# Kernel optimization log

Hardware: AMD Instinct MI355X
Metric: run time of the kernel (lower is better)

The kernel has to match this reference:

```python
import jax, jax.numpy as jnp
from jax import lax
import numpy as np

M_FILTERS = 128   # rows of responses D
N_CHANNELS = 1024 # cols of responses D (spectral channels)
BATCH = 4096
N_LAYERS = 17
IMAX = 50


def setup_inputs() -> dict:
    key = jax.random.key(0)
    k1, k2, k3, k4 = jax.random.split(key, 4)
    t1 = jax.random.normal(k1, (BATCH, N_CHANNELS), dtype=jnp.float32)
    t2 = jax.random.normal(k2, (BATCH, N_CHANNELS), dtype=jnp.float32)
    params = jax.random.uniform(k3, (M_FILTERS, N_LAYERS), dtype=jnp.float32)
    responses = jax.random.normal(k4, (M_FILTERS, N_CHANNELS), dtype=jnp.float32)
    return {
        "t1": t1,
        "t2": t2,
        "params": params,
        "thick_min": jnp.float32(0.0),
        "thick_max": jnp.float32(1.0),
        "beta_range": jnp.float32(0.1),
        "responses": responses,
    }


def _coherence_reduce(D0):
    """Faithful vectorized version of the 50-iteration coherence-reduction loop.

    The original per-row Python loop (Ri[i] > Rth branch) only reads row i and
    pre-computed Rth/delta, so it is exactly a masked row update.
    torch.linalg.eig on the symmetric matrices G is replaced by eigh (same
    eigenpairs up to sign/order; order is fixed by the explicit descending sort,
    and only the top-M eigenpairs reach the output D[:M,:]).
    """
    Mr, Nr = D0.shape
    ratio = jnp.float32(Nr / Mr)
    eye_b = jnp.eye(Nr, dtype=bool)

    def body(_, D):
        D = D / jnp.linalg.norm(D)                      # Frobenius norm over (0,1)
        G = D.T @ D                                     # [N, N]
        Sigma, V = jnp.linalg.eigh(G)
        Sigma = jnp.where(jnp.abs(Sigma) > 1e-10, ratio, Sigma)
        G = (V * Sigma[None, :]) @ V.T                  # V diag(Sigma) V^T
        G0 = jnp.abs(G - jnp.diag(jnp.diag(G)))
        Ri = jnp.sum(G0, axis=0)                        # [N]
        Rth = jnp.min(Ri)
        delta = Rth / (Nr - 1)
        mask = (Ri > Rth)[:, None]                      # rows to clip
        Gn = jnp.where(mask, delta * jnp.sign(G), G)
        Gn = jnp.where(eye_b, G, Gn)                    # keep original diagonal
        G = (Gn + Gn.T) * 0.5
        Sigma, V = jnp.linalg.eigh(G)
        order = jnp.argsort(-Sigma)                     # descending
        Sigma = Sigma[order]
        V = V[:, order]
        # Original: Sigma[M:-1]=0 then D = diag(Sigma)^{1/2} @ V.T, D = D[:M,:].
        # Only the top-M eigenpairs contribute to the first M rows.
        Dn = jnp.power(Sigma[:Mr], 0.5)[:, None] * V[:, :Mr].T  # [M, N]
        return Dn

    return lax.fori_loop(0, IMAX, body, D0)


def reference(t1, t2, params, thick_min, thick_max, beta_range, responses):
    # HybnetLoss: MSE match loss + hinge range loss (filter_loss is zeroed in source)
    match_loss = jnp.mean((t1 - t2) ** 2)
    d = jnp.float32(0.01)
    res = jnp.maximum((params - thick_min - d) / (-d),
                      (params - thick_max + d) / d)
    range_loss = jnp.mean(jnp.maximum(res, jnp.zeros_like(res)))
    original_loss = match_loss + beta_range * range_loss

    # HybnetLoss_plus: coherence-reduction regularizer on the response matrix
    D = _coherence_reduce(responses)
    rloss = jnp.mean((D - responses) ** 2)
    return original_loss + rloss
```

## Files before the change

kernel.cpp:

```cpp
#include <hip/hip_runtime.h>

#define NBLK 256
#define NTHR 512

#define OFF_G    0
#define OFF_QT   1048576
#define OFF_Y    1179648
#define OFF_C    1703936
#define OFF_RP   1851392
#define OFF_ACC  1867776
#define OFF_BAR  1867792

#define BAR_A 0
#define BAR_B 64
#define BAR_C 128
#define BAR_E 136

typedef float v4f __attribute__((ext_vector_type(4)));

__device__ __forceinline__ void cld4_8(v4f& a, v4f& b, v4f& c, v4f& d,
                                       v4f& e, v4f& f, v4f& g, v4f& h,
                                       const float* pa, const float* pb,
                                       const float* pc, const float* pd,
                                       const float* pe, const float* pf,
                                       const float* pg, const float* ph) {
    asm volatile("global_load_dwordx4 %0, %8, off sc1\n\t"
                 "global_load_dwordx4 %1, %9, off sc1\n\t"
                 "global_load_dwordx4 %2, %10, off sc1\n\t"
                 "global_load_dwordx4 %3, %11, off sc1\n\t"
                 "global_load_dwordx4 %4, %12, off sc1\n\t"
                 "global_load_dwordx4 %5, %13, off sc1\n\t"
                 "global_load_dwordx4 %6, %14, off sc1\n\t"
                 "global_load_dwordx4 %7, %15, off sc1\n\t"
                 "s_waitcnt vmcnt(0)"
                 : "=&v"(a), "=&v"(b), "=&v"(c), "=&v"(d),
                   "=&v"(e), "=&v"(f), "=&v"(g), "=&v"(h)
                 : "v"(pa), "v"(pb), "v"(pc), "v"(pd),
                   "v"(pe), "v"(pf), "v"(pg), "v"(ph) : "memory");
}
__device__ __forceinline__ void cld4_4(v4f& a, v4f& b, v4f& c, v4f& d,
                                       const float* pa, const float* pb,
                                       const float* pc, const float* pd) {
    asm volatile("global_load_dwordx4 %0, %4, off sc1\n\t"
                 "global_load_dwordx4 %1, %5, off sc1\n\t"
                 "global_load_dwordx4 %2, %6, off sc1\n\t"
                 "global_load_dwordx4 %3, %7, off sc1\n\t"
                 "s_waitcnt vmcnt(0)"
                 : "=&v"(a), "=&v"(b), "=&v"(c), "=&v"(d)
                 : "v"(pa), "v"(pb), "v"(pc), "v"(pd) : "memory");
}
__device__ __forceinline__ void cld4_2(v4f& a, v4f& b,
                                       const float* pa, const float* pb) {
    asm volatile("global_load_dwordx4 %0, %2, off sc1\n\t"
                 "global_load_dwordx4 %1, %3, off sc1\n\t"
                 "s_waitcnt vmcnt(0)"
                 : "=&v"(a), "=&v"(b) : "v"(pa), "v"(pb) : "memory");
}
__device__ __forceinline__ void cld1_4(float& a, float& b, float& c, float& d,
                                       const float* pa, const float* pb,
                                       const float* pc, const float* pd) {
    asm volatile("global_load_dword %0, %4, off sc1\n\t"
                 "global_load_dword %1, %5, off sc1\n\t"
                 "global_load_dword %2, %6, off sc1\n\t"
                 "global_load_dword %3, %7, off sc1\n\t"
                 "s_waitcnt vmcnt(0)"
                 : "=&v"(a), "=&v"(b), "=&v"(c), "=&v"(d)
                 : "v"(pa), "v"(pb), "v"(pc), "v"(pd) : "memory");
}
__device__ __forceinline__ void cld1_8(float& a, float& b, float& c, float& d,
                                       float& e, float& f, float& g, float& h,
                                       const float* pa, const float* pb,
                                       const float* pc, const float* pd,
                                       const float* pe, const float* pf,
                                       const float* pg, const float* ph) {
    asm volatile("global_load_dword %0, %8, off sc1\n\t"
                 "global_load_dword %1, %9, off sc1\n\t"
                 "global_load_dword %2, %10, off sc1\n\t"
                 "global_load_dword %3, %11, off sc1\n\t"
                 "global_load_dword %4, %12, off sc1\n\t"
                 "global_load_dword %5, %13, off sc1\n\t"
                 "global_load_dword %6, %14, off sc1\n\t"
                 "global_load_dword %7, %15, off sc1\n\t"
                 "s_waitcnt vmcnt(0)"
                 : "=&v"(a), "=&v"(b), "=&v"(c), "=&v"(d),
                   "=&v"(e), "=&v"(f), "=&v"(g), "=&v"(h)
                 : "v"(pa), "v"(pb), "v"(pc), "v"(pd),
                   "v"(pe), "v"(pf), "v"(pg), "v"(ph) : "memory");
}
__device__ __forceinline__ void iss2(v4f& a, v4f& b,
                                     const float* pa, const float* pb) {
    asm volatile("global_load_dwordx4 %0, %2, off sc1\n\t"
                 "global_load_dwordx4 %1, %3, off sc1"
                 : "=&v"(a), "=&v"(b) : "v"(pa), "v"(pb) : "memory");
}
__device__ __forceinline__ void wt2(v4f& a, v4f& b) {
    asm volatile("s_waitcnt vmcnt(0)" : "+v"(a), "+v"(b) :: "memory");
}
__device__ __forceinline__ void iss1(v4f& a, const float* pa) {
    asm volatile("global_load_dwordx4 %0, %1, off sc1"
                 : "=&v"(a) : "v"(pa) : "memory");
}
__device__ __forceinline__ void wt1(v4f& a) {
    asm volatile("s_waitcnt vmcnt(0)" : "+v"(a) :: "memory");
}

__device__ __forceinline__ void ast2(float* p, float a, float b) {
    union { unsigned long long u; float f[2]; } c; c.f[0] = a; c.f[1] = b;
    __hip_atomic_store((unsigned long long*)p, c.u,
                       __ATOMIC_RELAXED, __HIP_MEMORY_SCOPE_AGENT);
}
__device__ __forceinline__ float ald(const float* p) {
    return __hip_atomic_load(p, __ATOMIC_RELAXED, __HIP_MEMORY_SCOPE_AGENT);
}
__device__ __forceinline__ void ast(float* p, float x) {
    __hip_atomic_store(p, x, __ATOMIC_RELAXED, __HIP_MEMORY_SCOPE_AGENT);
}

__device__ __forceinline__ void bar_arrive(unsigned* bb, int line) {
    __syncthreads();
    if (threadIdx.x == 0)
        __hip_atomic_fetch_add(bb + line * 16, 1u,
                               __ATOMIC_RELAXED, __HIP_MEMORY_SCOPE_AGENT);
}
__device__ __forceinline__ void bar_wait(unsigned* bb, int wbase, int nlines,
                                         unsigned tgt) {
    if ((int)threadIdx.x < nlines) {
        while (__hip_atomic_load(bb + (wbase + threadIdx.x) * 16,
                                 __ATOMIC_RELAXED, __HIP_MEMORY_SCOPE_AGENT) < tgt)
            __builtin_amdgcn_s_sleep(1);
    }
    __builtin_amdgcn_s_waitcnt(0);
    __syncthreads();
}

union Smem {
    struct { float As[32][68]; float Bs[32][68]; float Rs[64][17]; } gg;
    struct { float Cs[128][129]; float inv_d[16]; float irs[128];
             float Xs[16][64]; } chol;
    struct { float Ri[1024]; float red[512]; float As[32][36]; float Bs[32][68]; } gy;
    struct { float As[32][68]; float Bs[32][68]; float red[512]; } tb;
    float red[512];
};

__device__ __forceinline__ void dev_match(Smem* sm, const float* t1, const float* t2,
                                          float* accb, int w) {
    int tid = threadIdx.x;
    const float4* a = (const float4*)t1;
    const float4* b = (const float4*)t2;
    float s = 0.f;
    for (int i = w * 512 + tid; i < 1048576; i += 218 * 512) {
        float4 x = a[i], y = b[i];
        float d0 = x.x - y.x, d1 = x.y - y.y, d2 = x.z - y.z, d3 = x.w - y.w;
        s += d0 * d0 + d1 * d1 + d2 * d2 + d3 * d3;
    }
    sm->red[tid] = s; __syncthreads();
    for (int w2 = 256; w2 > 0; w2 >>= 1) {
        if (tid < w2) sm->red[tid] += sm->red[tid + w2];
        __syncthreads();
    }
    if (tid == 0) atomicAdd(&accb[0], sm->red[0]);
    __syncthreads();
}

__device__ __forceinline__ void dev_range(Smem* sm, const float* params, const float* tmin,
                                          const float* tmax, float* accb) {
    int tid = threadIdx.x;
    float a = tmin[0], b = tmax[0];
    const float d = 0.01f;
    float s = 0.f;
    for (int i = tid; i < 128 * 17; i += 512) {
        float p = params[i];
        float r1 = (p - a - d) / (-d);
        float r2 = (p - b + d) / d;
        s += fmaxf(fmaxf(r1, r2), 0.f);
    }
    sm->red[tid] = s; __syncthreads();
    for (int w = 256; w > 0; w >>= 1) {
        if (tid < w) sm->red[tid] += sm->red[tid + w];
        __syncthreads();
    }
    if (tid == 0) atomicAdd(&accb[1], sm->red[0]);
    __syncthreads();
}

__device__ __forceinline__ void dev_sumsq(Smem* sm, const float* X, float* accb, int w) {
    int tid = threadIdx.x;
    float s = 0.f;
    for (int i = w * 512 + tid; i < 131072; i += 2048) { float v = X[i]; s += v * v; }
    sm->red[tid] = s; __syncthreads();
    for (int w2 = 256; w2 > 0; w2 >>= 1) {
        if (tid < w2) sm->red[tid] += sm->red[tid + w2];
        __syncthreads();
    }
    if (tid == 0) atomicAdd(&accb[3], sm->red[0]);
    __syncthreads();
}

__device__ __forceinline__ void dev_syrk(Smem* sm, const float* A, const float* B,
                                         float* C, int bid) {
    int tid = threadIdx.x;
    int q0 = (bid & 1) * 64, p0 = ((bid >> 1) & 1) * 64, z = bid >> 2;
    int kc0 = z * 128;
    int p = tid & 63, kg = (tid >> 6) * 4;
    int tx = tid & 15, ty = tid >> 4;
    float acc[2][4] = {};
    v4f av, bv;
    iss2(av, bv, &A[(p0 + p) * 1024 + kc0 + kg], &B[(q0 + p) * 1024 + kc0 + kg]);
    for (int ck = 0; ck < 4; ++ck) {
        wt2(av, bv);
        sm->gg.As[kg + 0][p] = av.x; sm->gg.As[kg + 1][p] = av.y;
        sm->gg.As[kg + 2][p] = av.z; sm->gg.As[kg + 3][p] = av.w;
        sm->gg.Bs[kg + 0][p] = bv.x; sm->gg.Bs[kg + 1][p] = bv.y;
        sm->gg.Bs[kg + 2][p] = bv.z; sm->gg.Bs[kg + 3][p] = bv.w;
        __syncthreads();
        if (ck < 3) {
            int kn = kc0 + (ck + 1) * 32 + kg;
            iss2(av, bv, &A[(p0 + p) * 1024 + kn], &B[(q0 + p) * 1024 + kn]);
        }
        for (int k = 0; k < 32; ++k) {
            float2 a2 = *(const float2*)&sm->gg.As[k][ty * 2];
            float4 b4 = *(const float4*)&sm->gg.Bs[k][tx * 4];
            acc[0][0] += a2.x * b4.x; acc[0][1] += a2.x * b4.y;
            acc[0][2] += a2.x * b4.z; acc[0][3] += a2.x * b4.w;
            acc[1][0] += a2.y * b4.x; acc[1][1] += a2.y * b4.y;
            acc[1][2] += a2.y * b4.z; acc[1][3] += a2.y * b4.w;
        }
        __syncthreads();
    }
    #pragma unroll
    for (int i = 0; i < 2; ++i)
        #pragma unroll
        for (int j = 0; j < 4; ++j)
            atomicAdd(&C[(p0 + ty * 2 + i) * 128 + q0 + tx * 4 + j], acc[i][j]);
}

__device__ __forceinline__ void dev_cholTrsm(Smem* sm, const float* C, const float* RHS,
                                             float* Qt, int bid) {
    int tid = threadIdx.x;
    {
        const float* base = C + tid * 32;
        v4f z0, z1, z2, z3, z4, z5, z6, z7;
        cld4_8(z0, z1, z2, z3, z4, z5, z6, z7,
               base, base + 4, base + 8, base + 12,
               base + 16, base + 20, base + 24, base + 28);
        int r = tid >> 2, c0 = (tid & 3) * 32;
        *(v4f*)&sm->chol.Cs[r][c0]      = z0; *(v4f*)&sm->chol.Cs[r][c0 + 4]  = z1;
        *(v4f*)&sm->chol.Cs[r][c0 + 8]  = z2; *(v4f*)&sm->chol.Cs[r][c0 + 12] = z3;
        *(v4f*)&sm->chol.Cs[r][c0 + 16] = z4; *(v4f*)&sm->chol.Cs[r][c0 + 20] = z5;
        *(v4f*)&sm->chol.Cs[r][c0 + 24] = z6; *(v4f*)&sm->chol.Cs[r][c0 + 28] = z7;
    }
    __syncthreads();
    int lane = tid & 63;
    for (int kb = 0; kb < 8; ++kb) {
        int k0 = kb * 16;
        if (tid < 64) {
            float P0[16], P1[16], invs[16];
            #pragma unroll
            for (int u = 0; u < 16; ++u) {
                P0[u] = sm->chol.Cs[lane][k0 + u];
                P1[u] = sm->chol.Cs[lane + 64][k0 + u];
            }
            #pragma unroll
            for (int kk = 0; kk < 16; ++kk) {
                int k = k0 + kk;
                int src = k & 63;
                bool hi = (k >= 64);
                float pr[16];
                #pragma unroll
                for (int u = 0; u < 16; ++u)
                    if (u >= kk) pr[u] = __shfl(hi ? P1[u] : P0[u], src);
                float inv = 1.0f / pr[kk];
                invs[kk] = inv;
                float f0 = (lane > k) ? P0[kk] * inv : 0.f;
                float f1 = ((lane + 64) > k) ? P1[kk] * inv : 0.f;
                #pragma unroll
                for (int u = kk + 1; u < 16; ++u) {
                    P0[u] -= f0 * pr[u];
                    P1[u] -= f1 * pr[u];
                }
            }
            #pragma unroll
            for (int u = 0; u < 16; ++u) {
                sm->chol.Cs[lane][k0 + u] = P0[u];
                sm->chol.Cs[lane + 64][k0 + u] = P1[u];
            }
            if (lane == 0) {
                #pragma unroll
                for (int kk = 0; kk < 16; ++kk) sm->chol.inv_d[kk] = invs[kk];
            }
        }
        __syncthreads();
        int base = k0 + 16;
        if (base < 128) {
            int hh = tid >> 6, cc = tid & 63;
            int j1 = base + cc;
            int j2 = base + cc + 64;
            bool has1 = (j1 < 128), has2 = (j2 < 128);
            float w1[16], w2[16];
            if (has1) {
                #pragma unroll
                for (int u = 0; u < 16; ++u) w1[u] = sm->chol.Cs[j1][k0 + u] * sm->chol.inv_d[u];
            }
            if (has2) {
                #pragma unroll
                for (int u = 0; u < 16; ++u) w2[u] = sm->chol.Cs[j2][k0 + u] * sm->chol.inv_d[u];
            }
            int rlo = hh * 16;
            int istart = rlo > base ? rlo : base;
            for (int i = istart; i < rlo + 16; ++i) {
                float v[16];
                #pragma unroll
                for (int u = 0; u < 16; ++u) v[u] = sm->chol.Cs[i][k0 + u];
                float a1 = 0.f, a2 = 0.f;
                #pragma unroll
                for (int u = 0; u < 16; ++u) { a1 += v[u] * w1[u]; a2 += v[u] * w2[u]; }
                if (has1) sm->chol.Cs[i][j1] -= a1;
                if (has2) sm->chol.Cs[i][j2] -= a2;
            }
        }
        __syncthreads();
    }
    if (tid < 128) sm->chol.irs[tid] = 1.0f / sqrtf(sm->chol.Cs[tid][tid]);
    int c = tid & 63, h = tid >> 6;
    int j0 = bid * 64;
    float acc[16];
    {
        const float* p = &RHS[(h * 16) * 1024 + j0 + c];
        cld1_8(acc[0], acc[1], acc[2], acc[3], acc[4], acc[5], acc[6], acc[7],
               p, p + 1024, p + 2048, p + 3072, p + 4096, p + 5120, p + 6144, p + 7168);
        cld1_8(acc[8], acc[9], acc[10], acc[11], acc[12], acc[13], acc[14], acc[15],
               p + 8192, p + 9216, p + 10240, p + 11264,
               p + 12288, p + 13312, p + 14336, p + 15360);
    }
    __syncthreads();
    for (int pb = 0; pb < 8; ++pb) {
        int p0 = pb * 16;
        if (h == pb) {
            #pragma unroll
            for (int kk = 0; kk < 16; ++kk) {
                int k = p0 + kk;
                float irsk = sm->chol.irs[k];
                float x = acc[kk] * irsk;
                acc[kk] = x;
                sm->chol.Xs[kk][c] = x;
                float xs = x * irsk;
                #pragma unroll
                for (int r = kk + 1; r < 16; ++r)
                    acc[r] -= sm->chol.Cs[p0 + r][k] * xs;
            }
        }
        __syncthreads();
        if (h > pb) {
            int rb = h * 16;
            #pragma unroll
            for (int kk = 0; kk < 16; ++kk) {
                int k = p0 + kk;
                float xs = sm->chol.Xs[kk][c] * sm->chol.irs[k];
                #pragma unroll
                for (int r = 0; r < 16; ++r)
                    acc[r] -= sm->chol.Cs[rb + r][k] * xs;
            }
        }
        __syncthreads();
    }
    #pragma unroll
    for (int r = 0; r < 16; ++r)
        ast(&Qt[(h * 16 + r) * 1024 + j0 + c], acc[r]);
}

__device__ __forceinline__ void dev_gemmG(Smem* sm, const float* Qt, float* G,
                                          float* Rpart, int bid) {
    int tid = threadIdx.x;
    int tx = tid & 15, ty = tid >> 4;
    int bx = bid & 15, by = bid >> 4;
    int a0 = by * 64, b0 = bx * 64;
    int r0 = tid >> 4, c4 = (tid & 15) << 2;
    float acc[2][4] = {};
    v4f av, bv;
    iss2(av, bv, &Qt[r0 * 1024 + a0 + c4], &Qt[r0 * 1024 + b0 + c4]);
    for (int kc = 0; kc < 128; kc += 32) {
        wt2(av, bv);
        *(v4f*)&sm->gg.As[r0][c4] = av;
        *(v4f*)&sm->gg.Bs[r0][c4] = bv;
        __syncthreads();
        if (kc < 96) {
            int kn = kc + 32;
            iss2(av, bv, &Qt[(kn + r0) * 1024 + a0 + c4],
                 &Qt[(kn + r0) * 1024 + b0 + c4]);
        }
        for (int k = 0; k < 32; ++k) {
            float2 a2 = *(const float2*)&sm->gg.As[k][ty * 2];
            float4 b4 = *(const float4*)&sm->gg.Bs[k][tx * 4];
            acc[0][0] += a2.x * b4.x; acc[0][1] += a2.x * b4.y;
            acc[0][2] += a2.x * b4.z; acc[0][3] += a2.x * b4.w;
            acc[1][0] += a2.y * b4.x; acc[1][1] += a2.y * b4.y;
            acc[1][2] += a2.y * b4.z; acc[1][3] += a2.y * b4.w;
        }
        __syncthreads();
    }
    float rsum[2] = {0.f, 0.f};
    #pragma unroll
    for (int i = 0; i < 2; ++i) {
        int aa = a0 + ty * 2 + i;
        float g[4];
        #pragma unroll
        for (int j = 0; j < 4; ++j) g[j] = 8.f * acc[i][j];
        float* gp = &G[aa * 1024 + b0 + tx * 4];
        ast2(gp, g[0], g[1]);
        ast2(gp + 2, g[2], g[3]);
        int bb = b0 + tx * 4;
        #pragma unroll
        for (int j = 0; j < 4; ++j) rsum[i] += (aa == bb + j) ? 0.f : fabsf(g[j]);
    }
    sm->gg.Rs[ty * 2 + 0][tx] = rsum[0];
    sm->gg.Rs[ty * 2 + 1][tx] = rsum[1];
    __syncthreads();
    if (tid < 64) {
        float s = 0.f;
        #pragma unroll
        for (int x = 0; x < 16; ++x) s += sm->gg.Rs[tid][x];
        ast(&Rpart[(a0 + tid) * 16 + bx], s);
    }
}

__device__ __forceinline__ void dev_ri(Smem* sm, const float* Rpart,
                                       float* rth, float* delta) {
    int tid = threadIdx.x;
    int e0 = tid, e1 = tid + 512;
    v4f t0, t1, t2, t3, u0, u1, u2, u3;
    cld4_8(t0, t1, t2, t3, u0, u1, u2, u3,
           &Rpart[e0 * 16], &Rpart[e0 * 16 + 4],
           &Rpart[e0 * 16 + 8], &Rpart[e0 * 16 + 12],
           &Rpart[e1 * 16], &Rpart[e1 * 16 + 4],
           &Rpart[e1 * 16 + 8], &Rpart[e1 * 16 + 12]);
    float s0 = 0.f;
    s0 += t0.x; s0 += t0.y; s0 += t0.z; s0 += t0.w;
    s0 += t1.x; s0 += t1.y; s0 += t1.z; s0 += t1.w;
    s0 += t2.x; s0 += t2.y; s0 += t2.z; s0 += t2.w;
    s0 += t3.x; s0 += t3.y; s0 += t3.z; s0 += t3.w;
    float s1 = 0.f;
    s1 += u0.x; s1 += u0.y; s1 += u0.z; s1 += u0.w;
    s1 += u1.x; s1 += u1.y; s1 += u1.z; s1 += u1.w;
    s1 += u2.x; s1 += u2.y; s1 += u2.z; s1 += u2.w;
    s1 += u3.x; s1 += u3.y; s1 += u3.z; s1 += u3.w;
    sm->gy.Ri[e0] = s0;
    sm->gy.Ri[e1] = s1;
    float mn = fminf(s0, s1);
    #pragma unroll
    for (int off = 32; off > 0; off >>= 1)
        mn = fminf(mn, __shfl_xor(mn, off));
    if ((tid & 63) == 0) sm->gy.red[tid >> 6] = mn;
    __syncthreads();
    float r = sm->gy.red[0];
    #pragma unroll
    for (int w = 1; w < 8; ++w) r = fminf(r, sm->gy.red[w]);
    *rth = r;
    *delta = r / 1023.f;
}

__device__ __forceinline__ void dev_gemmY(Smem* sm, const float* Qt, const float* G,
                                          float rth, float delta, float* Y, int bid) {
    int tid = threadIdx.x;
    int j0 = (bid & 15) * 64;
    int m0 = ((bid >> 4) & 3) * 32;
    int kz = bid >> 6;
    int kc0 = kz * 256;
    int tx = tid & 15, ty = tid >> 4;
    int m = (tid & 255) >> 3, k4 = (tid & 7) << 2;
    int rg = tid >> 4, cg = (tid & 15) << 2;
    float acc[4] = {};
    v4f q, g0;
    if (tid < 256) iss1(q, &Qt[(m0 + m) * 1024 + kc0 + k4]);
    iss1(g0, &G[(kc0 + rg) * 1024 + j0 + cg]);
    for (int kc = kc0; kc < kc0 + 256; kc += 32) {
        wt1(g0);
        if (tid < 256) {
            wt1(q);
            *(v4f*)&sm->gy.As[m][k4] = q;
        }
        {
            int a = kc + rg;
            float ria = sm->gy.Ri[a];
            v4f bw;
            #pragma unroll
            for (int u = 0; u < 4; ++u) {
                int b = j0 + cg + u;
                float g = g0[u];
                float sg = delta * ((g > 0.f) ? 1.f : ((g < 0.f) ? -1.f : 0.f));
                float ga = (ria > rth) ? sg : g;
                float gb = (sm->gy.Ri[b] > rth) ? sg : g;
                bw[u] = (a == b) ? g : 0.5f * (ga + gb);
            }
            *(v4f*)&sm->gy.Bs[rg][cg] = bw;
        }
        __syncthreads();
        if (kc < kc0 + 224) {
            int kn = kc + 32;
            if (tid < 256) iss1(q, &Qt[(m0 + m) * 1024 + kn + k4]);
            iss1(g0, &G[(kn + rg) * 1024 + j0 + cg]);
        }
        #pragma unroll
        for (int kb = 0; kb < 8; ++kb) {
            v4f qa = *(const v4f*)&sm->gy.As[ty][kb * 4];
            #pragma unroll
            for (int kk = 0; kk < 4; ++kk) {
                float4 b4 = *(const float4*)&sm->gy.Bs[kb * 4 + kk][tx * 4];
                float a = qa[kk];
                acc[0] += a * b4.x; acc[1] += a * b4.y;
                acc[2] += a * b4.z; acc[3] += a * b4.w;
            }
        }
        __syncthreads();
    }
    #pragma unroll
    for (int j = 0; j < 4; ++j)
        atomicAdd(&Y[(m0 + ty) * 1024 + j0 + tx * 4 + j], acc[j]);
}

__device__ __forceinline__ void dev_trB(Smem* sm, const float* Qt, const float* G,
                                        const float* Rpart, float* accb, int bid) {
    int tid = threadIdx.x;
    float rth, delta;
    dev_ri(sm, Rpart, &rth, &delta);
    __syncthreads();
    int tx = tid & 15, ty = tid >> 4;
    int a0 = (bid >> 4) * 64, b0 = (bid & 15) * 64;
    int r0 = tid >> 4, c4 = (tid & 15) << 2;
    float acc[2][4] = {};
    for (int kc = 0; kc < 128; kc += 32) {
        v4f av, bv;
        cld4_2(av, bv, &Qt[(kc + r0) * 1024 + a0 + c4],
               &Qt[(kc + r0) * 1024 + b0 + c4]);
        *(v4f*)&sm->tb.As[r0][c4] = av;
        *(v4f*)&sm->tb.Bs[r0][c4] = bv;
        __syncthreads();
        for (int k = 0; k < 32; ++k) {
            float2 a2 = *(const float2*)&sm->tb.As[k][ty * 2];
            float4 b4 = *(const float4*)&sm->tb.Bs[k][tx * 4];
            acc[0][0] += a2.x * b4.x; acc[0][1] += a2.x * b4.y;
            acc[0][2] += a2.x * b4.z; acc[0][3] += a2.x * b4.w;
            acc[1][0] += a2.y * b4.x; acc[1][1] += a2.y * b4.y;
            acc[1][2] += a2.y * b4.z; acc[1][3] += a2.y * b4.w;
        }
        __syncthreads();
    }
    float rib[4];
    #pragma unroll
    for (int j = 0; j < 4; ++j) {
        int bb = b0 + tx * 4 + j;
        v4f t0, t1, t2, t3;
        cld4_4(t0, t1, t2, t3, &Rpart[bb * 16], &Rpart[bb * 16 + 4],
               &Rpart[bb * 16 + 8], &Rpart[bb * 16 + 12]);
        float s = 0.f;
        s += t0.x; s += t0.y; s += t0.z; s += t0.w;
        s += t1.x; s += t1.y; s += t1.z; s += t1.w;
        s += t2.x; s += t2.y; s += t2.z; s += t2.w;
        s += t3.x; s += t3.y; s += t3.z; s += t3.w;
        rib[j] = s;
    }
    float s = 0.f;
    #pragma unroll
    for (int i = 0; i < 2; ++i) {
        int aa = a0 + ty * 2 + i;
        v4f t0, t1, t2, t3;
        cld4_4(t0, t1, t2, t3, &Rpart[aa * 16], &Rpart[aa * 16 + 4],
               &Rpart[aa * 16 + 8], &Rpart[aa * 16 + 12]);
        float ria = 0.f;
        ria += t0.x; ria += t0.y; ria += t0.z; ria += t0.w;
        ria += t1.x; ria += t1.y; ria += t1.z; ria += t1.w;
        ria += t2.x; ria += t2.y; ria += t2.z; ria += t2.w;
        ria += t3.x; ria += t3.y; ria += t3.z; ria += t3.w;
        float g0, g1, g2, g3;
        const float* gp = &G[aa * 1024 + b0 + tx * 4];
        cld1_4(g0, g1, g2, g3, gp, gp + 1, gp + 2, gp + 3);
        float gv[4] = {g0, g1, g2, g3};
        #pragma unroll
        for (int j = 0; j < 4; ++j) {
            int bb = b0 + tx * 4 + j;
            float g = gv[j];
            float sg = delta * ((g > 0.f) ? 1.f : ((g < 0.f) ? -1.f : 0.f));
            float ga = (ria > rth) ? sg : g;
            float gb = (rib[j] > rth) ? sg : g;
            float gp2 = (aa == bb) ? g : 0.5f * (ga + gb);
            s += gp2 * acc[i][j];
        }
    }
    __syncthreads();
    sm->tb.red[tid] = s;
    __syncthreads();
    for (int w = 256; w > 0; w >>= 1) {
        if (tid < w) sm->tb.red[tid] += sm->tb.red[tid + w];
        __syncthreads();
    }
    if (tid == 0) atomicAdd(&accb[2], sm->tb.red[0]);
}

__global__ __launch_bounds__(512) void mega(const float* __restrict__ t1,
                                            const float* __restrict__ t2,
                                            const float* __restrict__ params,
                                            const float* __restrict__ tmin,
                                            const float* __restrict__ tmax,
                                            const float* __restrict__ beta,
                                            const float* __restrict__ R,
                                            float* ws, float* out) {
    float* G     = ws + OFF_G;
    float* Qt    = ws + OFF_QT;
    float* Y     = ws + OFF_Y;
    float* C     = ws + OFF_C;
    float* Rpart = ws + OFF_RP;
    float* accb  = ws + OFF_ACC;
    unsigned* bb = (unsigned*)(ws + OFF_BAR);
    __shared__ Smem sm;
    int bid = blockIdx.x;
    int tid = threadIdx.x;
    unsigned phA = 0, phB = 0, phC = 0, phE = 0;

    if (bid < 32) {
        ast(&C[bid * 512 + tid], 0.f);
    } else if (bid < 250) dev_match(&sm, t1, t2, accb, bid - 32);
    else if (bid == 250) dev_range(&sm, params, tmin, tmax, accb);
    else if (bid < 255) dev_sumsq(&sm, R, accb, bid - 251);
    ++phC;
    if (bid < 32) {
        bar_arrive(bb, BAR_C + (bid >> 2));
        bar_wait(bb, BAR_C, 8, phC * 4);
        dev_syrk(&sm, R, R, C, bid);
    }
    ++phC;
    if (bid < 32) bar_arrive(bb, BAR_C + (bid >> 2));
    if (bid < 16) {
        bar_wait(bb, BAR_C, 8, phC * 4);
        dev_cholTrsm(&sm, C, R, Qt, bid);
    }
    ++phE;
    if (bid < 16) bar_arrive(bb, BAR_E + (bid >> 2));
    bar_wait(bb, BAR_E, 4, phE * 4);

    for (int it = 0; it < 50; ++it) {
        dev_gemmG(&sm, Qt, G, Rpart, bid);
        ast(&Y[bid * 512 + tid], 0.f);
        if (bid < 32) ast(&C[bid * 512 + tid], 0.f);
        ++phA;
        bar_arrive(bb, BAR_A + (bid & 63));
        bar_wait(bb, BAR_A, 64, phA * 4);
        {
            float rth, delta;
            dev_ri(&sm, Rpart, &rth, &delta);
            dev_gemmY(&sm, Qt, G, rth, delta, Y, bid);
        }
        ++phB;
        bar_arrive(bb, BAR_B + (bid & 63));
        if (bid < 32) {
            bar_wait(bb, BAR_B, 64, phB * 4);
            dev_syrk(&sm, Y, Y, C, bid);
        }
        ++phC;
        if (bid < 32) bar_arrive(bb, BAR_C + (bid >> 2));
        if (bid < 16) {
            bar_wait(bb, BAR_C, 8, phC * 4);
            dev_cholTrsm(&sm, C, Y, Qt, bid);
        }
        ++phE;
        if (bid < 16) bar_arrive(bb, BAR_E + (bid >> 2));
        bar_wait(bb, BAR_E, 4, phE * 4);
    }

    dev_trB(&sm, Qt, G, Rpart, accb, bid);
    ++phA;
    bar_arrive(bb, BAR_A + (bid & 63));
    if (bid == 0) {
        bar_wait(bb, BAR_A, 64, phA * 4);
        if (tid == 0)
            out[0] = ald(&accb[0]) / 4194304.f + beta[0] * (ald(&accb[1]) / 2176.f)
                   + (ald(&accb[2]) + ald(&accb[3])) / 131072.f;
    }
}

extern "C" void kernel_launch(void* const* d_in, const int* in_sizes, int n_in,
                              void* d_out, int out_size, void* d_ws, size_t ws_size,
                              hipStream_t stream) {
    const float* t1 = (const float*)d_in[0];
    const float* t2 = (const float*)d_in[1];
    const float* params = (const float*)d_in[2];
    const float* tmin = (const float*)d_in[3];
    const float* tmax = (const float*)d_in[4];
    const float* beta = (const float*)d_in[5];
    const float* R = (const float*)d_in[6];
    float* ws = (float*)d_ws;
    float* out = (float*)d_out;

    hipMemsetAsync(ws + OFF_ACC, 0, 9280, stream);
    mega<<<NBLK, NTHR, 0, stream>>>(t1, t2, params, tmin, tmax, beta, R, ws, out);
}
```

Measured before the change: 7.340 ms.

## Deepen load pipelining with double-buffered LDS and overlap Cholesky panel with updates

The syrk, gemmG and gemmY device phases now issue all four or more K-chunk global loads up front and wait on them with partial vmcnt counts. They also double-buffer the LDS tiles so that one barrier per chunk replaces two. The blocked Cholesky is restructured: the next panel factorization by wave 0 overlaps the trailing update done by the other waves, and the RHS loads are issued before factorization and waited on later. The change also uses fast rcp/rsq intrinsics and a lighter LDS-only barrier. Costs are higher register pressure and LDS footprint, plus some precision loss from the approximate reciprocals.

```diff
diff --git a/kernel.cpp b/kernel.cpp
--- a/kernel.cpp
+++ b/kernel.cpp
@@ -17,6 +17,7 @@
 #define BAR_E 136
 
 typedef float v4f __attribute__((ext_vector_type(4)));
+typedef float v2f __attribute__((ext_vector_type(2)));
 
 __device__ __forceinline__ void cld4_8(v4f& a, v4f& b, v4f& c, v4f& d,
                                        v4f& e, v4f& f, v4f& g, v4f& h,
@@ -67,12 +68,24 @@
                  : "=&v"(a), "=&v"(b), "=&v"(c), "=&v"(d)
                  : "v"(pa), "v"(pb), "v"(pc), "v"(pd) : "memory");
 }
-__device__ __forceinline__ void cld1_8(float& a, float& b, float& c, float& d,
-                                       float& e, float& f, float& g, float& h,
-                                       const float* pa, const float* pb,
-                                       const float* pc, const float* pd,
-                                       const float* pe, const float* pf,
-                                       const float* pg, const float* ph) {
+__device__ __forceinline__ void iss2(v4f& a, v4f& b,
+                                     const float* pa, const float* pb) {
+    asm volatile("global_load_dwordx4 %0, %2, off sc1\n\t"
+                 "global_load_dwordx4 %1, %3, off sc1"
+                 : "=&v"(a), "=&v"(b) : "v"(pa), "v"(pb) : "memory");
+}
+__device__ __forceinline__ void issY(v2f& q, v4f& g,
+                                     const float* pq, const float* pg) {
+    asm volatile("global_load_dwordx2 %0, %2, off sc1\n\t"
+                 "global_load_dwordx4 %1, %3, off sc1"
+                 : "=&v"(q), "=&v"(g) : "v"(pq), "v"(pg) : "memory");
+}
+__device__ __forceinline__ void issS8(float& a, float& b, float& c, float& d,
+                                      float& e, float& f, float& g, float& h,
+                                      const float* pa, const float* pb,
+                                      const float* pc, const float* pd,
+                                      const float* pe, const float* pf,
+                                      const float* pg, const float* ph) {
     asm volatile("global_load_dword %0, %8, off sc1\n\t"
                  "global_load_dword %1, %9, off sc1\n\t"
                  "global_load_dword %2, %10, off sc1\n\t"
@@ -80,28 +93,39 @@
                  "global_load_dword %4, %12, off sc1\n\t"
                  "global_load_dword %5, %13, off sc1\n\t"
                  "global_load_dword %6, %14, off sc1\n\t"
-                 "global_load_dword %7, %15, off sc1\n\t"
-                 "s_waitcnt vmcnt(0)"
+                 "global_load_dword %7, %15, off sc1"
                  : "=&v"(a), "=&v"(b), "=&v"(c), "=&v"(d),
                    "=&v"(e), "=&v"(f), "=&v"(g), "=&v"(h)
                  : "v"(pa), "v"(pb), "v"(pc), "v"(pd),
                    "v"(pe), "v"(pf), "v"(pg), "v"(ph) : "memory");
 }
-__device__ __forceinline__ void iss2(v4f& a, v4f& b,
-                                     const float* pa, const float* pb) {
-    asm volatile("global_load_dwordx4 %0, %2, off sc1\n\t"
-                 "global_load_dwordx4 %1, %3, off sc1"
-                 : "=&v"(a), "=&v"(b) : "v"(pa), "v"(pb) : "memory");
-}
-__device__ __forceinline__ void wt2(v4f& a, v4f& b) {
-    asm volatile("s_waitcnt vmcnt(0)" : "+v"(a), "+v"(b) :: "memory");
-}
-__device__ __forceinline__ void iss1(v4f& a, const float* pa) {
-    asm volatile("global_load_dwordx4 %0, %1, off sc1"
-                 : "=&v"(a) : "v"(pa) : "memory");
-}
-__device__ __forceinline__ void wt1(v4f& a) {
-    asm volatile("s_waitcnt vmcnt(0)" : "+v"(a) :: "memory");
+#define DEF_WT2(NAME, NSTR) \
+__device__ __forceinline__ void NAME(v4f& a, v4f& b) { \
+    asm volatile("s_waitcnt vmcnt(" NSTR ")" : "+v"(a), "+v"(b) :: "memory"); }
+DEF_WT2(wt2_6, "6")
+DEF_WT2(wt2_4, "4")
+DEF_WT2(wt2_2, "2")
+DEF_WT2(wt2_0, "0")
+#define DEF_WTY(NAME, NSTR) \
+__device__ __forceinline__ void NAME(v2f& q, v4f& g) { \
+    asm volatile("s_waitcnt vmcnt(" NSTR ")" : "+v"(q), "+v"(g) :: "memory"); }
+DEF_WTY(wtY_6, "6")
+DEF_WTY(wtY_4, "4")
+DEF_WTY(wtY_2, "2")
+DEF_WTY(wtY_0, "0")
+__device__ __forceinline__ void wtA16(float* a) {
+    asm volatile("s_waitcnt vmcnt(0)"
+                 : "+v"(a[0]), "+v"(a[1]), "+v"(a[2]), "+v"(a[3]),
+                   "+v"(a[4]), "+v"(a[5]), "+v"(a[6]), "+v"(a[7]),
+                   "+v"(a[8]), "+v"(a[9]), "+v"(a[10]), "+v"(a[11]),
+                   "+v"(a[12]), "+v"(a[13]), "+v"(a[14]), "+v"(a[15])
+                 :: "memory");
+}
+
+__device__ __forceinline__ void syncL() {
+    asm volatile("s_waitcnt lgkmcnt(0)" ::: "memory");
+    __builtin_amdgcn_s_barrier();
+    asm volatile("" ::: "memory");
 }
 
 __device__ __forceinline__ void ast2(float* p, float a, float b) {
@@ -134,10 +158,11 @@
 }
 
 union Smem {
-    struct { float As[32][68]; float Bs[32][68]; float Rs[64][17]; } gg;
-    struct { float Cs[128][129]; float inv_d[16]; float irs[128];
+    struct { float As[2][32][68]; float Bs[2][32][68]; float Rs[64][17]; } gg;
+    struct { float Cs[128][129]; float inv_d[2][16]; float irs[128];
              float Xs[16][64]; } chol;
-    struct { float Ri[1024]; float red[512]; float As[32][36]; float Bs[32][68]; } gy;
+    struct { float Ri[1024]; float red[512]; float As[2][32][36];
+             float Bs[2][32][68]; } gy;
     struct { float As[32][68]; float Bs[32][68]; float red[512]; } tb;
     float red[512];
 };
@@ -196,6 +221,23 @@
     __syncthreads();
 }
 
+#define SY_BODY(CK, RA, RB, WT) do { \
+    WT; \
+    sm->gg.As[(CK) & 1][kg + 0][p] = RA.x; sm->gg.As[(CK) & 1][kg + 1][p] = RA.y; \
+    sm->gg.As[(CK) & 1][kg + 2][p] = RA.z; sm->gg.As[(CK) & 1][kg + 3][p] = RA.w; \
+    sm->gg.Bs[(CK) & 1][kg + 0][p] = RB.x; sm->gg.Bs[(CK) & 1][kg + 1][p] = RB.y; \
+    sm->gg.Bs[(CK) & 1][kg + 2][p] = RB.z; sm->gg.Bs[(CK) & 1][kg + 3][p] = RB.w; \
+    syncL(); \
+    for (int k = 0; k < 32; ++k) { \
+        float2 a2 = *(const float2*)&sm->gg.As[(CK) & 1][k][ty * 2]; \
+        float4 b4 = *(const float4*)&sm->gg.Bs[(CK) & 1][k][tx * 4]; \
+        acc[0][0] += a2.x * b4.x; acc[0][1] += a2.x * b4.y; \
+        acc[0][2] += a2.x * b4.z; acc[0][3] += a2.x * b4.w; \
+        acc[1][0] += a2.y * b4.x; acc[1][1] += a2.y * b4.y; \
+        acc[1][2] += a2.y * b4.z; acc[1][3] += a2.y * b4.w; \
+    } \
+} while (0)
+
 __device__ __forceinline__ void dev_syrk(Smem* sm, const float* A, const float* B,
                                          float* C, int bid) {
     int tid = threadIdx.x;
@@ -204,34 +246,60 @@
     int p = tid & 63, kg = (tid >> 6) * 4;
     int tx = tid & 15, ty = tid >> 4;
     float acc[2][4] = {};
-    v4f av, bv;
-    iss2(av, bv, &A[(p0 + p) * 1024 + kc0 + kg], &B[(q0 + p) * 1024 + kc0 + kg]);
-    for (int ck = 0; ck < 4; ++ck) {
-        wt2(av, bv);
-        sm->gg.As[kg + 0][p] = av.x; sm->gg.As[kg + 1][p] = av.y;
-        sm->gg.As[kg + 2][p] = av.z; sm->gg.As[kg + 3][p] = av.w;
-        sm->gg.Bs[kg + 0][p] = bv.x; sm->gg.Bs[kg + 1][p] = bv.y;
-        sm->gg.Bs[kg + 2][p] = bv.z; sm->gg.Bs[kg + 3][p] = bv.w;
-        __syncthreads();
-        if (ck < 3) {
-            int kn = kc0 + (ck + 1) * 32 + kg;
-            iss2(av, bv, &A[(p0 + p) * 1024 + kn], &B[(q0 + p) * 1024 + kn]);
-        }
-        for (int k = 0; k < 32; ++k) {
-            float2 a2 = *(const float2*)&sm->gg.As[k][ty * 2];
-            float4 b4 = *(const float4*)&sm->gg.Bs[k][tx * 4];
-            acc[0][0] += a2.x * b4.x; acc[0][1] += a2.x * b4.y;
-            acc[0][2] += a2.x * b4.z; acc[0][3] += a2.x * b4.w;
-            acc[1][0] += a2.y * b4.x; acc[1][1] += a2.y * b4.y;
-            acc[1][2] += a2.y * b4.z; acc[1][3] += a2.y * b4.w;
-        }
-        __syncthreads();
-    }
+    v4f a0r, b0r, a1r, b1r, a2r, b2r, a3r, b3r;
+    const float* Ab = &A[(p0 + p) * 1024 + kc0 + kg];
+    const float* Bb = &B[(q0 + p) * 1024 + kc0 + kg];
+    iss2(a0r, b0r, Ab, Bb);
+    iss2(a1r, b1r, Ab + 32, Bb + 32);
+    iss2(a2r, b2r, Ab + 64, Bb + 64);
+    iss2(a3r, b3r, Ab + 96, Bb + 96);
+    SY_BODY(0, a0r, b0r, wt2_6(a0r, b0r));
+    SY_BODY(1, a1r, b1r, wt2_4(a1r, b1r));
+    SY_BODY(2, a2r, b2r, wt2_2(a2r, b2r));
+    SY_BODY(3, a3r, b3r, wt2_0(a3r, b3r));
     #pragma unroll
     for (int i = 0; i < 2; ++i)
         #pragma unroll
         for (int j = 0; j < 4; ++j)
             atomicAdd(&C[(p0 + ty * 2 + i) * 128 + q0 + tx * 4 + j], acc[i][j]);
+}
+
+__device__ __forceinline__ void chol_panel(Smem* sm, int kb, int lane) {
+    int k0 = kb * 16;
+    float P0[16], P1[16], invs[16];
+    #pragma unroll
+    for (int u = 0; u < 16; ++u) {
+        P0[u] = sm->chol.Cs[lane][k0 + u];
+        P1[u] = sm->chol.Cs[lane + 64][k0 + u];
+    }
+    #pragma unroll
+    for (int kk = 0; kk < 16; ++kk) {
+        int k = k0 + kk;
+        int src = k & 63;
+        bool hi = (k >= 64);
+        float pr[16];
+        #pragma unroll
+        for (int u = 0; u < 16; ++u)
+            if (u >= kk) pr[u] = __shfl(hi ? P1[u] : P0[u], src);
+        float inv = __builtin_amdgcn_rcpf(pr[kk]);
+        invs[kk] = inv;
+        float f0 = (lane > k) ? P0[kk] * inv : 0.f;
+        float f1 = ((lane + 64) > k) ? P1[kk] * inv : 0.f;
+        #pragma unroll
+        for (int u = kk + 1; u < 16; ++u) {
+            P0[u] -= f0 * pr[u];
+            P1[u] -= f1 * pr[u];
+        }
+    }
+    #pragma unroll
+    for (int u = 0; u < 16; ++u) {
+        sm->chol.Cs[lane][k0 + u] = P0[u];
+        sm->chol.Cs[lane + 64][k0 + u] = P1[u];
+    }
+    if (lane == 0) {
+        #pragma unroll
+        for (int kk = 0; kk < 16; ++kk) sm->chol.inv_d[kb & 1][kk] = invs[kk];
+    }
 }
 
 __device__ __forceinline__ void dev_cholTrsm(Smem* sm, const float* C, const float* RHS,
@@ -249,90 +317,73 @@
         *(v4f*)&sm->chol.Cs[r][c0 + 16] = z4; *(v4f*)&sm->chol.Cs[r][c0 + 20] = z5;
         *(v4f*)&sm->chol.Cs[r][c0 + 24] = z6; *(v4f*)&sm->chol.Cs[r][c0 + 28] = z7;
     }
-    __syncthreads();
-    int lane = tid & 63;
-    for (int kb = 0; kb < 8; ++kb) {
-        int k0 = kb * 16;
-        if (tid < 64) {
-            float P0[16], P1[16], invs[16];
-            #pragma unroll
-            for (int u = 0; u < 16; ++u) {
-                P0[u] = sm->chol.Cs[lane][k0 + u];
-                P1[u] = sm->chol.Cs[lane + 64][k0 + u];
-            }
-            #pragma unroll
-            for (int kk = 0; kk < 16; ++kk) {
-                int k = k0 + kk;
-                int src = k & 63;
-                bool hi = (k >= 64);
-                float pr[16];
-                #pragma unroll
-                for (int u = 0; u < 16; ++u)
-                    if (u >= kk) pr[u] = __shfl(hi ? P1[u] : P0[u], src);
-                float inv = 1.0f / pr[kk];
-                invs[kk] = inv;
-                float f0 = (lane > k) ? P0[kk] * inv : 0.f;
-                float f1 = ((lane + 64) > k) ? P1[kk] * inv : 0.f;
-                #pragma unroll
-                for (int u = kk + 1; u < 16; ++u) {
-                    P0[u] -= f0 * pr[u];
-                    P1[u] -= f1 * pr[u];
-                }
-            }
-            #pragma unroll
-            for (int u = 0; u < 16; ++u) {
-                sm->chol.Cs[lane][k0 + u] = P0[u];
-                sm->chol.Cs[lane + 64][k0 + u] = P1[u];
-            }
-            if (lane == 0) {
-                #pragma unroll
-                for (int kk = 0; kk < 16; ++kk) sm->chol.inv_d[kk] = invs[kk];
-            }
-        }
-        __syncthreads();
-        int base = k0 + 16;
-        if (base < 128) {
-            int hh = tid >> 6, cc = tid & 63;
-            int j1 = base + cc;
-            int j2 = base + cc + 64;
-            bool has1 = (j1 < 128), has2 = (j2 < 128);
-            float w1[16], w2[16];
-            if (has1) {
-                #pragma unroll
-                for (int u = 0; u < 16; ++u) w1[u] = sm->chol.Cs[j1][k0 + u] * sm->chol.inv_d[u];
-            }
-            if (has2) {
-                #pragma unroll
-                for (int u = 0; u < 16; ++u) w2[u] = sm->chol.Cs[j2][k0 + u] * sm->chol.inv_d[u];
-            }
-            int rlo = hh * 16;
-            int istart = rlo > base ? rlo : base;
-            for (int i = istart; i < rlo + 16; ++i) {
-                float v[16];
-                #pragma unroll
-                for (int u = 0; u < 16; ++u) v[u] = sm->chol.Cs[i][k0 + u];
-                float a1 = 0.f, a2 = 0.f;
-                #pragma unroll
-                for (int u = 0; u < 16; ++u) { a1 += v[u] * w1[u]; a2 += v[u] * w2[u]; }
-                if (has1) sm->chol.Cs[i][j1] -= a1;
-                if (has2) sm->chol.Cs[i][j2] -= a2;
-            }
-        }
-        __syncthreads();
-    }
-    if (tid < 128) sm->chol.irs[tid] = 1.0f / sqrtf(sm->chol.Cs[tid][tid]);
+    syncL();
     int c = tid & 63, h = tid >> 6;
     int j0 = bid * 64;
     float acc[16];
     {
-        const float* p = &RHS[(h * 16) * 1024 + j0 + c];
-        cld1_8(acc[0], acc[1], acc[2], acc[3], acc[4], acc[5], acc[6], acc[7],
-               p, p + 1024, p + 2048, p + 3072, p + 4096, p + 5120, p + 6144, p + 7168);
-        cld1_8(acc[8], acc[9], acc[10], acc[11], acc[12], acc[13], acc[14], acc[15],
-               p + 8192, p + 9216, p + 10240, p + 11264,
-               p + 12288, p + 13312, p + 14336, p + 15360);
-    }
-    __syncthreads();
+        const float* pRHS = &RHS[(h * 16) * 1024 + j0 + c];
+        issS8(acc[0], acc[1], acc[2], acc[3], acc[4], acc[5], acc[6], acc[7],
+              pRHS, pRHS + 1024, pRHS + 2048, pRHS + 3072,
+              pRHS + 4096, pRHS + 5120, pRHS + 6144, pRHS + 7168);
+        issS8(acc[8], acc[9], acc[10], acc[11], acc[12], acc[13], acc[14], acc[15],
+              pRHS + 8192, pRHS + 9216, pRHS + 10240, pRHS + 11264,
+              pRHS + 12288, pRHS + 13312, pRHS + 14336, pRHS + 15360);
+    }
+    int lane = tid & 63;
+    if (tid < 64) chol_panel(sm, 0, lane);
+    syncL();
+    for (int kb = 0; kb < 7; ++kb) {
+        int k0 = kb * 16, base = k0 + 16;
+        const float* idp = sm->chol.inv_d[kb & 1];
+        int hh = tid >> 6, cc = tid & 63;
+        int rlo = hh * 16;
+        if (cc < 16 && rlo + 16 > base) {
+            int j1 = base + cc;
+            float w1[16];
+            #pragma unroll
+            for (int u = 0; u < 16; ++u) w1[u] = sm->chol.Cs[j1][k0 + u] * idp[u];
+            int istart = rlo > base ? rlo : base;
+            for (int i = istart; i < rlo + 16; ++i) {
+                float a1 = 0.f;
+                #pragma unroll
+                for (int u = 0; u < 16; ++u) a1 += sm->chol.Cs[i][k0 + u] * w1[u];
+                sm->chol.Cs[i][j1] -= a1;
+            }
+        }
+        syncL();
+        if (tid < 64) {
+            chol_panel(sm, kb + 1, lane);
+        } else if (rlo + 16 > base) {
+            int b2 = base + 16;
+            int j1 = b2 + cc, j2 = b2 + cc + 64;
+            bool has1 = j1 < 128, has2 = j2 < 128;
+            if (has1) {
+                float w1[16], w2[16];
+                #pragma unroll
+                for (int u = 0; u < 16; ++u) w1[u] = sm->chol.Cs[j1][k0 + u] * idp[u];
+                if (has2) {
+                    #pragma unroll
+                    for (int u = 0; u < 16; ++u) w2[u] = sm->chol.Cs[j2][k0 + u] * idp[u];
+                }
+                int istart = rlo > base ? rlo : base;
+                for (int i = istart; i < rlo + 16; ++i) {
+                    float a1 = 0.f, a2 = 0.f;
+                    #pragma unroll
+                    for (int u = 0; u < 16; ++u) {
+                        float v = sm->chol.Cs[i][k0 + u];
+                        a1 += v * w1[u]; a2 += v * w2[u];
+                    }
+                    sm->chol.Cs[i][j1] -= a1;
+                    if (has2) sm->chol.Cs[i][j2] -= a2;
+                }
+            }
+        }
+        syncL();
+    }
+    if (tid < 128) sm->chol.irs[tid] = __builtin_amdgcn_rsqf(sm->chol.Cs[tid][tid]);
+    wtA16(acc);
+    syncL();
     for (int pb = 0; pb < 8; ++pb) {
         int p0 = pb * 16;
         if (h == pb) {
@@ -349,7 +400,7 @@
                     acc[r] -= sm->chol.Cs[p0 + r][k] * xs;
             }
         }
-        __syncthreads();
+        syncL();
         if (h > pb) {
             int rb = h * 16;
             #pragma unroll
@@ -361,12 +412,27 @@
                     acc[r] -= sm->chol.Cs[rb + r][k] * xs;
             }
         }
-        __syncthreads();
+        syncL();
     }
     #pragma unroll
     for (int r = 0; r < 16; ++r)
         ast(&Qt[(h * 16 + r) * 1024 + j0 + c], acc[r]);
 }
+
+#define GG_BODY(CK, RA, RB, WT) do { \
+    WT; \
+    *(v4f*)&sm->gg.As[(CK) & 1][r0][c4] = RA; \
+    *(v4f*)&sm->gg.Bs[(CK) & 1][r0][c4] = RB; \
+    syncL(); \
+    for (int k = 0; k < 32; ++k) { \
+        float2 a2 = *(const float2*)&sm->gg.As[(CK) & 1][k][ty * 2]; \
+        float4 b4 = *(const float4*)&sm->gg.Bs[(CK) & 1][k][tx * 4]; \
+        acc[0][0] += a2.x * b4.x; acc[0][1] += a2.x * b4.y; \
+        acc[0][2] += a2.x * b4.z; acc[0][3] += a2.x * b4.w; \
+        acc[1][0] += a2.y * b4.x; acc[1][1] += a2.y * b4.y; \
+        acc[1][2] += a2.y * b4.z; acc[1][3] += a2.y * b4.w; \
+    } \
+} while (0)
 
 __device__ __forceinline__ void dev_gemmG(Smem* sm, const float* Qt, float* G,
                                           float* Rpart, int bid) {
@@ -376,28 +442,17 @@
     int a0 = by * 64, b0 = bx * 64;
     int r0 = tid >> 4, c4 = (tid & 15) << 2;
     float acc[2][4] = {};
-    v4f av, bv;
-    iss2(av, bv, &Qt[r0 * 1024 + a0 + c4], &Qt[r0 * 1024 + b0 + c4]);
-    for (int kc = 0; kc < 128; kc += 32) {
-        wt2(av, bv);
-        *(v4f*)&sm->gg.As[r0][c4] = av;
-        *(v4f*)&sm->gg.Bs[r0][c4] = bv;
-        __syncthreads();
-        if (kc < 96) {
-            int kn = kc + 32;
-            iss2(av, bv, &Qt[(kn + r0) * 1024 + a0 + c4],
-                 &Qt[(kn + r0) * 1024 + b0 + c4]);
-        }
-        for (int k = 0; k < 32; ++k) {
-            float2 a2 = *(const float2*)&sm->gg.As[k][ty * 2];
-            float4 b4 = *(const float4*)&sm->gg.Bs[k][tx * 4];
-            acc[0][0] += a2.x * b4.x; acc[0][1] += a2.x * b4.y;
-            acc[0][2] += a2.x * b4.z; acc[0][3] += a2.x * b4.w;
-            acc[1][0] += a2.y * b4.x; acc[1][1] += a2.y * b4.y;
-            acc[1][2] += a2.y * b4.z; acc[1][3] += a2.y * b4.w;
-        }
-        __syncthreads();
-    }
+    v4f a0r, b0r, a1r, b1r, a2r, b2r, a3r, b3r;
+    const float* pa = &Qt[r0 * 1024 + a0 + c4];
+    const float* pb = &Qt[r0 * 1024 + b0 + c4];
+    iss2(a0r, b0r, pa, pb);
+    iss2(a1r, b1r, pa + 32 * 1024, pb + 32 * 1024);
+    iss2(a2r, b2r, pa + 64 * 1024, pb + 64 * 1024);
+    iss2(a3r, b3r, pa + 96 * 1024, pb + 96 * 1024);
+    GG_BODY(0, a0r, b0r, wt2_6(a0r, b0r));
+    GG_BODY(1, a1r, b1r, wt2_4(a1r, b1r));
+    GG_BODY(2, a2r, b2r, wt2_2(a2r, b2r));
+    GG_BODY(3, a3r, b3r, wt2_0(a3r, b3r));
     float rsum[2] = {0.f, 0.f};
     #pragma unroll
     for (int i = 0; i < 2; ++i) {
@@ -414,7 +469,7 @@
     }
     sm->gg.Rs[ty * 2 + 0][tx] = rsum[0];
     sm->gg.Rs[ty * 2 + 1][tx] = rsum[1];
-    __syncthreads();
+    syncL();
     if (tid < 64) {
         float s = 0.f;
         #pragma unroll
@@ -450,13 +505,46 @@
     for (int off = 32; off > 0; off >>= 1)
         mn = fminf(mn, __shfl_xor(mn, off));
     if ((tid & 63) == 0) sm->gy.red[tid >> 6] = mn;
-    __syncthreads();
+    syncL();
     float r = sm->gy.red[0];
     #pragma unroll
     for (int w = 1; w < 8; ++w) r = fminf(r, sm->gy.red[w]);
     *rth = r;
     *delta = r / 1023.f;
 }
+
+#define GY_BODY(CK, RQ, RG, WT, REISSUE) do { \
+    WT; \
+    *(v2f*)&sm->gy.As[(CK) & 1][mA][k2] = RQ; \
+    { \
+        int aIdx = kc0 + (CK) * 32 + rg; \
+        float ria = sm->gy.Ri[aIdx]; \
+        v4f bw; \
+        _Pragma("unroll") \
+        for (int u = 0; u < 4; ++u) { \
+            int bIdx = j0 + cg + u; \
+            float g = RG[u]; \
+            float sg = delta * ((g > 0.f) ? 1.f : ((g < 0.f) ? -1.f : 0.f)); \
+            float ga = (ria > rth) ? sg : g; \
+            float gb = (sm->gy.Ri[bIdx] > rth) ? sg : g; \
+            bw[u] = (aIdx == bIdx) ? g : 0.5f * (ga + gb); \
+        } \
+        *(v4f*)&sm->gy.Bs[(CK) & 1][rg][cg] = bw; \
+    } \
+    syncL(); \
+    REISSUE; \
+    _Pragma("unroll") \
+    for (int kb = 0; kb < 8; ++kb) { \
+        v4f qa = *(const v4f*)&sm->gy.As[(CK) & 1][ty][kb * 4]; \
+        _Pragma("unroll") \
+        for (int kk = 0; kk < 4; ++kk) { \
+            float4 b4 = *(const float4*)&sm->gy.Bs[(CK) & 1][kb * 4 + kk][tx * 4]; \
+            float av = qa[kk]; \
+            acc[0] += av * b4.x; acc[1] += av * b4.y; \
+            acc[2] += av * b4.z; acc[3] += av * b4.w; \
+        } \
+    } \
+} while (0)
 
 __device__ __forceinline__ void dev_gemmY(Smem* sm, const float* Qt, const float* G,
                                           float rth, float delta, float* Y, int bid) {
@@ -466,52 +554,25 @@
     int kz = bid >> 6;
     int kc0 = kz * 256;
     int tx = tid & 15, ty = tid >> 4;
-    int m = (tid & 255) >> 3, k4 = (tid & 7) << 2;
+    int mA = tid >> 4, k2 = (tid & 15) << 1;
     int rg = tid >> 4, cg = (tid & 15) << 2;
     float acc[4] = {};
-    v4f q, g0;
-    if (tid < 256) iss1(q, &Qt[(m0 + m) * 1024 + kc0 + k4]);
-    iss1(g0, &G[(kc0 + rg) * 1024 + j0 + cg]);
-    for (int kc = kc0; kc < kc0 + 256; kc += 32) {
-        wt1(g0);
-        if (tid < 256) {
-            wt1(q);
-            *(v4f*)&sm->gy.As[m][k4] = q;
-        }
-        {
-            int a = kc + rg;
-            float ria = sm->gy.Ri[a];
-            v4f bw;
-            #pragma unroll
-            for (int u = 0; u < 4; ++u) {
-                int b = j0 + cg + u;
-                float g = g0[u];
-                float sg = delta * ((g > 0.f) ? 1.f : ((g < 0.f) ? -1.f : 0.f));
-                float ga = (ria > rth) ? sg : g;
-                float gb = (sm->gy.Ri[b] > rth) ? sg : g;
-                bw[u] = (a == b) ? g : 0.5f * (ga + gb);
-            }
-            *(v4f*)&sm->gy.Bs[rg][cg] = bw;
-        }
-        __syncthreads();
-        if (kc < kc0 + 224) {
-            int kn = kc + 32;
-            if (tid < 256) iss1(q, &Qt[(m0 + m) * 1024 + kn + k4]);
-            iss1(g0, &G[(kn + rg) * 1024 + j0 + cg]);
-        }
-        #pragma unroll
-        for (int kb = 0; kb < 8; ++kb) {
-            v4f qa = *(const v4f*)&sm->gy.As[ty][kb * 4];
-            #pragma unroll
-            for (int kk = 0; kk < 4; ++kk) {
-                float4 b4 = *(const float4*)&sm->gy.Bs[kb * 4 + kk][tx * 4];
-                float a = qa[kk];
-                acc[0] += a * b4.x; acc[1] += a * b4.y;
-                acc[2] += a * b4.z; acc[3] += a * b4.w;
-            }
-        }
-        __syncthreads();
-    }
+    v2f q0r, q1r, q2r, q3r;
+    v4f g0r, g1r, g2r, g3r;
+    const float* pq = &Qt[(m0 + mA) * 1024 + kc0 + k2];
+    const float* pg = &G[(kc0 + rg) * 1024 + j0 + cg];
+    issY(q0r, g0r, pq, pg);
+    issY(q1r, g1r, pq + 32, pg + 32 * 1024);
+    issY(q2r, g2r, pq + 64, pg + 64 * 1024);
+    issY(q3r, g3r, pq + 96, pg + 96 * 1024);
+    GY_BODY(0, q0r, g0r, wtY_6(q0r, g0r), issY(q0r, g0r, pq + 128, pg + 128 * 1024));
+    GY_BODY(1, q1r, g1r, wtY_6(q1r, g1r), issY(q1r, g1r, pq + 160, pg + 160 * 1024));
+    GY_BODY(2, q2r, g2r, wtY_6(q2r, g2r), issY(q2r, g2r, pq + 192, pg + 192 * 1024));
+    GY_BODY(3, q3r, g3r, wtY_6(q3r, g3r), issY(q3r, g3r, pq + 224, pg + 224 * 1024));
+    GY_BODY(4, q0r, g0r, wtY_6(q0r, g0r), (void)0);
+    GY_BODY(5, q1r, g1r, wtY_4(q1r, g1r), (void)0);
+    GY_BODY(6, q2r, g2r, wtY_2(q2r, g2r), (void)0);
+    GY_BODY(7, q3r, g3r, wtY_0(q3r, g3r), (void)0);
     #pragma unroll
     for (int j = 0; j < 4; ++j)
         atomicAdd(&Y[(m0 + ty) * 1024 + j0 + tx * 4 + j], acc[j]);
```

New measurement: 27.05 ms. 3.69x slower.
